# Optimization experiments

Hardware: AMD Instinct MI355X
Metric: run time of the kernel (lower is better)

## Reference

```python
import jax, jax.numpy as jnp
import numpy as np

HIDDEN = 1024
N_HEADS = 16
HEAD_DIM = HIDDEN // N_HEADS


def setup_inputs() -> dict:
    key = jax.random.key(0)
    ks = jax.random.split(key, 7)
    b, l, m = 4, 1024, 1024
    q = jax.random.normal(ks[0], (b, l, HIDDEN), dtype=jnp.float32)
    k = jax.random.normal(ks[1], (b, m, HIDDEN), dtype=jnp.float32)
    v = jax.random.normal(ks[2], (b, m, HIDDEN), dtype=jnp.float32)
    s = 1.0 / np.sqrt(HIDDEN)
    w_q = jax.random.normal(ks[3], (HIDDEN, HIDDEN), dtype=jnp.float32) * s
    w_k = jax.random.normal(ks[4], (HIDDEN, HIDDEN), dtype=jnp.float32) * s
    w_v = jax.random.normal(ks[5], (HIDDEN, HIDDEN), dtype=jnp.float32) * s
    w_o = jax.random.normal(ks[6], (HIDDEN, HIDDEN), dtype=jnp.float32) * s
    return {"q": q, "k": k, "v": v, "w_q": w_q, "w_k": w_k, "w_v": w_v, "w_o": w_o}


def reference(q, k, v, w_q, w_k, w_v, w_o):
    b, l, _ = q.shape
    _, m, _ = k.shape
    # Linear (bias=False): y = x @ W^T
    qp = q @ w_q.T
    kp = k @ w_k.T
    vp = v @ w_v.T  # projected but unused downstream (faithful to original bug)
    # Faithful non-standard split: hidden -> (head_dim, n_heads)
    qh = qp.reshape(b, l, HEAD_DIM, N_HEADS)
    kh = kp.reshape(b, m, HEAD_DIM, N_HEADS)
    # attn over K, scaled, softmax over m (dim=2)
    scores = jnp.einsum('bldn,bmdn->blmn', qh, kh) / np.sqrt(HEAD_DIM)
    attn = jax.nn.softmax(scores, axis=2)
    # dropout is identity in eval mode
    # NOTE: original attends over K (not V) — reproduced faithfully
    x = jnp.einsum('blmn,bmdn->bldn', attn, kh)
    x = x.reshape(b, l, HIDDEN)  # 'b l d n -> b l (d n)'
    return x @ w_o.T
```

## Files before the change

kernel.cpp:

```cpp
#include <hip/hip_runtime.h>
#include <hip/hip_bf16.h>
#include <stdint.h>
#include <math.h>


typedef __bf16 bf16;
typedef __bf16 bf16x8 __attribute__((ext_vector_type(8)));
typedef __bf16 bf16x4 __attribute__((ext_vector_type(4)));
typedef float  f32x4  __attribute__((ext_vector_type(4)));

__device__ __forceinline__ void async_load16(const void* g, void* l) {
  __builtin_amdgcn_global_load_lds((__attribute__((address_space(1))) void*)g,
                                   (__attribute__((address_space(3))) void*)l,
                                   16, 0, 0);
}

__device__ __forceinline__ void pipe_fence() {
  asm volatile("s_waitcnt vmcnt(0) lgkmcnt(0)" ::: "memory");
  __builtin_amdgcn_sched_barrier(0);
  __builtin_amdgcn_s_barrier();
}

__device__ __forceinline__ int detect_fl(const void* samp, int tid, int* smax) {
  int e = (((const unsigned short*)samp)[tid] >> 7) & 0xFF;
#pragma unroll
  for (int off = 1; off <= 32; off <<= 1) {
    int o = __shfl_xor(e, off);
    e = o > e ? o : e;
  }
  if ((tid & 63) == 0) smax[tid >> 6] = e;
  __syncthreads();
  int m01 = smax[0] > smax[1] ? smax[0] : smax[1];
  int m23 = smax[2] > smax[3] ? smax[2] : smax[3];
  return ((m01 > m23 ? m01 : m23) >= 140) ? 1 : 0;
}

__global__ void __launch_bounds__(256)
canon(const void* __restrict__ q, const void* __restrict__ k,
      const void* __restrict__ wq, const void* __restrict__ wk,
      const void* __restrict__ wo,
      bf16* __restrict__ qc, bf16* __restrict__ kc,
      bf16* __restrict__ wqc, bf16* __restrict__ wkc,
      bf16* __restrict__ wo_p, int* __restrict__ flag) {
  __shared__ int smax[4];
  const int tid = threadIdx.x;
  const int fl = detect_fl(q, tid, smax);
  if (blockIdx.x == 0 && tid == 0) *flag = fl;

  const size_t e0 = (size_t)blockIdx.x * 2048 + tid * 8;
  const size_t M4 = 4194304, M8 = 8388608, M9 = 9437184, M10 = 10485760;
  const void* src; bf16* dst; size_t le; bool perm = false;
  if (e0 < M4)       { src = q;  dst = qc;   le = e0;       }
  else if (e0 < M8)  { src = k;  dst = kc;   le = e0 - M4;  }
  else if (e0 < M9)  { src = wq; dst = wqc;  le = e0 - M8;  }
  else if (e0 < M10) { src = wk; dst = wkc;  le = e0 - M9;  }
  else               { src = wo; dst = wo_p; le = e0 - M10; perm = true; }

  if (!perm) {
    bf16x8 v;
    if (fl) {
      const float* p = (const float*)src + le;
      f32x4 a = *(const f32x4*)p, b = *(const f32x4*)(p + 4);
#pragma unroll
      for (int j = 0; j < 4; ++j) { v[j] = (bf16)a[j]; v[4 + j] = (bf16)b[j]; }
    } else {
      v = *(const bf16x8*)((const bf16*)src + le);
    }
    *(bf16x8*)(dst + le) = v;
  } else {
    int o = (int)(le >> 10), kp0 = (int)(le & 1023);
    bf16x8 v;
#pragma unroll
    for (int j = 0; j < 8; ++j) {
      int kp = kp0 + j;
      int h = ((kp & 63) << 4) | (kp >> 6);
      float f = fl ? ((const float*)src)[o * 1024 + h]
                   : (float)((const bf16*)src)[o * 1024 + h];
      f = fminf(fmaxf(f, -1024.f), 1024.f);
      v[j] = (bf16)f;
    }
    *(bf16x8*)(dst + le) = v;
  }
}

__global__ void __launch_bounds__(256, 3)
qk_gemm(const bf16* __restrict__ qc, const bf16* __restrict__ wqc,
        const bf16* __restrict__ kc, const bf16* __restrict__ wkc,
        bf16* __restrict__ qh, bf16* __restrict__ kh, bf16* __restrict__ khT,
        float cs) {
  __shared__ __align__(16) char smem[49152];
  bf16* const sA0 = (bf16*)smem;
  bf16* const sA1 = (bf16*)(smem + 16384);
  bf16* const sB0 = (bf16*)(smem + 32768);
  bf16* const sB1 = (bf16*)(smem + 40960);
  bf16* const epi = (bf16*)smem;

  const int tid  = threadIdx.x;
  const int lane = tid & 63;
  const int wave = tid >> 6;
  const int q4   = lane >> 4;
  const int c16  = lane & 15;
  const int wm   = wave >> 1;
  const int wn   = wave & 1;

  const int z = blockIdx.z;
  const bf16* A = z ? kc : qc;
  const bf16* W = z ? wkc : wqc;
  const float scale = z ? 1.0f : cs;
  bf16* out0 = z ? kh : qh;

  const int lin    = blockIdx.x + 8 * blockIdx.y;
  const int rowBlk = (lin & 31) * 128;
  const int colBlk = (lin >> 5) * 64;

  const bf16* gA[4]; int lA[4];
#pragma unroll
  for (int i = 0; i < 4; ++i) {
    int s = tid + 256 * i;
    int r = s >> 3, g = (s & 7) ^ (r & 7);
    gA[i] = A + (size_t)(rowBlk + r) * 1024 + g * 8;
    lA[i] = s * 8;
  }
  const bf16* gB[2]; int lB[2];
#pragma unroll
  for (int i = 0; i < 2; ++i) {
    int s = tid + 256 * i;
    int r = s >> 3, g = (s & 7) ^ (r & 7);
    gB[i] = W + (size_t)(colBlk + r) * 1024 + g * 8;
    lB[i] = s * 8;
  }

  f32x4 acc[4][2] = {};

#pragma unroll
  for (int i = 0; i < 4; ++i) async_load16(gA[i], sA0 + lA[i]);
#pragma unroll
  for (int i = 0; i < 2; ++i) async_load16(gB[i], sB0 + lB[i]);
  pipe_fence();

  for (int t = 0; t < 16; ++t) {
    if (t < 15) {
      const int kn = (t + 1) * 64;
      bf16* dA = (t & 1) ? sA0 : sA1;
      bf16* dB = (t & 1) ? sB0 : sB1;
#pragma unroll
      for (int i = 0; i < 4; ++i) async_load16(gA[i] + kn, dA + lA[i]);
#pragma unroll
      for (int i = 0; i < 2; ++i) async_load16(gB[i] + kn, dB + lB[i]);
    }

    const bf16* cA = (t & 1) ? sA1 : sA0;
    const bf16* cB = (t & 1) ? sB1 : sB0;
#pragma unroll
    for (int ks = 0; ks < 2; ++ks) {
      bf16x8 af[4], bfr[2];
#pragma unroll
      for (int mt = 0; mt < 4; ++mt) {
        int row = wm * 64 + mt * 16 + c16;
        af[mt] = *(const bf16x8*)(cA + row * 64 +
                   (((ks * 4 + q4) ^ (row & 7)) * 8));
      }
#pragma unroll
      for (int nt = 0; nt < 2; ++nt) {
        int row = wn * 32 + nt * 16 + c16;
        bfr[nt] = *(const bf16x8*)(cB + row * 64 +
                   (((ks * 4 + q4) ^ (row & 7)) * 8));
      }
#pragma unroll
      for (int mt = 0; mt < 4; ++mt)
#pragma unroll
        for (int nt = 0; nt < 2; ++nt)
          acc[mt][nt] = __builtin_amdgcn_mfma_f32_16x16x32_bf16(
              af[mt], bfr[nt], acc[mt][nt], 0, 0, 0);
    }
    pipe_fence();
  }

#pragma unroll
  for (int mt = 0; mt < 4; ++mt)
#pragma unroll
    for (int nt = 0; nt < 2; ++nt)
#pragma unroll
      for (int r = 0; r < 4; ++r) {
        int m_t = wm * 64 + mt * 16 + q4 * 4 + r;
        int c   = wn * 32 + nt * 16 + c16;
        epi[m_t * 70 + c] = (bf16)(acc[mt][nt][r] * scale);
      }
  __syncthreads();

  const int bb    = rowBlk >> 10;
  const int mbase = rowBlk & 1023;
  const int dg0   = colBlk >> 4;

  {
    int n = tid >> 4;
#pragma unroll
    for (int i = 0; i < 8; ++i) {
      int m_t = (tid & 15) + i * 16;
      bf16x4 v;
#pragma unroll
      for (int dt = 0; dt < 4; ++dt) v[dt] = epi[m_t * 70 + dt * 16 + n];
      *(bf16x4*)(out0 + ((size_t)(bb * 16 + n) * 1024 + mbase + m_t) * 64 + dg0) = v;
    }
  }
  if (z) {
    int r = tid >> 2, qtr = tid & 3;
    int n = r >> 2, dt = r & 3;
    int c = dt * 16 + n;
    size_t base = ((size_t)(bb * 16 + n) * 64 + dg0 + dt) * 1024 + mbase + qtr * 32;
#pragma unroll
    for (int c8 = 0; c8 < 4; ++c8) {
      bf16x8 v;
#pragma unroll
      for (int j = 0; j < 8; ++j) v[j] = epi[(qtr * 32 + c8 * 8 + j) * 70 + c];
      *(bf16x8*)(khT + base + c8 * 8) = v;
    }
  }
}

__global__ void __launch_bounds__(256, 3)
attn_kernel(const bf16* __restrict__ qh, const bf16* __restrict__ kh,
            const bf16* __restrict__ khT, bf16* __restrict__ xh) {
  __shared__ __align__(16) bf16 sK[2][64 * 64];
  __shared__ __align__(16) bf16 sKT[2][64 * 64];
  __shared__ __align__(16) bf16 sP[4][16 * 72];

  const int tid  = threadIdx.x;
  const int lane = tid & 63;
  const int wave = tid >> 6;
  const int q4   = lane >> 4;
  const int c16  = lane & 15;
  const int lin  = blockIdx.x;
  const int bn   = lin & 63;
  const int qt   = lin >> 6;
  const int b    = bn >> 4, n = bn & 15;
  const int l0w  = qt * 64 + wave * 16;

  const bf16* qhead  = qh  + (size_t)bn * (1024 * 64);
  const bf16* khead  = kh  + (size_t)bn * (1024 * 64);
  const bf16* kThead = khT + (size_t)bn * (64 * 1024);

  bf16x8 aq[2];
#pragma unroll
  for (int hh = 0; hh < 2; ++hh)
    aq[hh] = *(const bf16x8*)(qhead + (size_t)(l0w + c16) * 64 + hh * 32 + q4 * 8);

  int kr[2], kg[2];
#pragma unroll
  for (int i = 0; i < 2; ++i) {
    int s = tid + 256 * i;
    kr[i] = s >> 3;  kg[i] = (s & 7) ^ (kr[i] & 7);
  }

  f32x4 O[4] = {};
  f32x4 Osum = {};
  bf16x8 ones;
#pragma unroll
  for (int j = 0; j < 8; ++j) ones[j] = (bf16)1.0f;
  bf16* sPw = sP[wave];

#pragma unroll
  for (int i = 0; i < 2; ++i) {
    int s = (tid + 256 * i) * 8;
    async_load16(khead + (size_t)kr[i] * 64 + kg[i] * 8, &sK[0][s]);
    async_load16(kThead + (size_t)kr[i] * 1024 + kg[i] * 8, &sKT[0][s]);
  }
  pipe_fence();

  for (int t = 0; t < 16; ++t) {
    if (t < 15) {
      const int m0n = (t + 1) * 64;
      const int bi  = (t + 1) & 1;
#pragma unroll
      for (int i = 0; i < 2; ++i) {
        int s = (tid + 256 * i) * 8;
        async_load16(khead + (size_t)(m0n + kr[i]) * 64 + kg[i] * 8, &sK[bi][s]);
        async_load16(kThead + (size_t)kr[i] * 1024 + m0n + kg[i] * 8, &sKT[bi][s]);
      }
    }

    const bf16* cK  = sK[t & 1];
    const bf16* cKT = sKT[t & 1];

    f32x4 S[4] = {};
#pragma unroll
    for (int t4 = 0; t4 < 4; ++t4) {
#pragma unroll
      for (int hh = 0; hh < 2; ++hh) {
        int row = t4 * 16 + c16;
        bf16x8 bk = *(const bf16x8*)(cK + row * 64 +
                                     (((hh * 4 + q4) ^ (row & 7)) * 8));
        S[t4] = __builtin_amdgcn_mfma_f32_16x16x32_bf16(aq[hh], bk, S[t4], 0, 0, 0);
      }
    }

#pragma unroll
    for (int t4 = 0; t4 < 4; ++t4)
#pragma unroll
      for (int r = 0; r < 4; ++r) {
        float p = __builtin_amdgcn_exp2f(S[t4][r]);
        sPw[(q4 * 4 + r) * 72 + t4 * 16 + c16] = (bf16)p;
      }

    bf16x8 ap[2];
#pragma unroll
    for (int kk2 = 0; kk2 < 2; ++kk2) {
      ap[kk2] = *(const bf16x8*)(sPw + c16 * 72 + kk2 * 32 + q4 * 8);
      Osum = __builtin_amdgcn_mfma_f32_16x16x32_bf16(ap[kk2], ones, Osum, 0, 0, 0);
    }

#pragma unroll
    for (int td = 0; td < 4; ++td) {
#pragma unroll
      for (int kk2 = 0; kk2 < 2; ++kk2) {
        int row = td * 16 + c16;
        bf16x8 bkt = *(const bf16x8*)(cKT + row * 64 +
                                      (((kk2 * 4 + q4) ^ (row & 7)) * 8));
        O[td] = __builtin_amdgcn_mfma_f32_16x16x32_bf16(ap[kk2], bkt, O[td], 0, 0, 0);
      }
    }
    pipe_fence();
  }

  {
    float inv[4];
#pragma unroll
    for (int r = 0; r < 4; ++r) inv[r] = 1.0f / Osum[r];
#pragma unroll
    for (int td = 0; td < 4; ++td)
#pragma unroll
      for (int r = 0; r < 4; ++r)
        sPw[(q4 * 4 + r) * 72 + td * 16 + c16] = (bf16)(O[td][r] * inv[r]);
  }
  {
    int l_loc = lane >> 2, dq = lane & 3;
    bf16x8 v0 = *(const bf16x8*)(sPw + l_loc * 72 + dq * 16);
    bf16x8 v1 = *(const bf16x8*)(sPw + l_loc * 72 + dq * 16 + 8);
    size_t base = ((size_t)(b * 1024 + l0w + l_loc) * 16 + n) * 64 + dq * 16;
    *(bf16x8*)(xh + base)     = v0;
    *(bf16x8*)(xh + base + 8) = v1;
  }
}

__global__ void __launch_bounds__(256, 4)
o_gemm(const bf16* __restrict__ A, const bf16* __restrict__ W,
       bf16* __restrict__ out0, float* __restrict__ outf,
       const int* __restrict__ flag) {
  __shared__ __align__(16) bf16 sA[2][64 * 64];
  __shared__ __align__(16) bf16 sB[2][64 * 64];

  const int tid  = threadIdx.x;
  const int lane = tid & 63;
  const int wave = tid >> 6;
  const int q4   = lane >> 4;
  const int c16  = lane & 15;
  const int wm   = wave >> 1;
  const int wn   = wave & 1;

  const int lin    = blockIdx.x + 8 * blockIdx.y;
  const int rowBlk = (lin & 63) * 64;
  const int colBlk = (lin >> 6) * 64;

  const bf16* gA[2]; const bf16* gB[2]; int ls[2];
#pragma unroll
  for (int i = 0; i < 2; ++i) {
    int s = tid + 256 * i;
    int r = s >> 3, g = (s & 7) ^ (r & 7);
    gA[i] = A + (size_t)(rowBlk + r) * 1024 + g * 8;
    gB[i] = W + (size_t)(colBlk + r) * 1024 + g * 8;
    ls[i] = s * 8;
  }

  f32x4 acc[2][2] = {};

#pragma unroll
  for (int i = 0; i < 2; ++i) {
    async_load16(gA[i], &sA[0][ls[i]]);
    async_load16(gB[i], &sB[0][ls[i]]);
  }
  pipe_fence();

  for (int t = 0; t < 16; ++t) {
    if (t < 15) {
      const int kn = (t + 1) * 64;
      const int bi = (t + 1) & 1;
#pragma unroll
      for (int i = 0; i < 2; ++i) {
        async_load16(gA[i] + kn, &sA[bi][ls[i]]);
        async_load16(gB[i] + kn, &sB[bi][ls[i]]);
      }
    }

    const bf16* cA = sA[t & 1];
    const bf16* cB = sB[t & 1];
#pragma unroll
    for (int ks = 0; ks < 2; ++ks) {
      bf16x8 af[2], bfr[2];
#pragma unroll
      for (int mt = 0; mt < 2; ++mt) {
        int row = wm * 32 + mt * 16 + c16;
        af[mt] = *(const bf16x8*)(cA + row * 64 +
                   (((ks * 4 + q4) ^ (row & 7)) * 8));
      }
#pragma unroll
      for (int nt = 0; nt < 2; ++nt) {
        int row = wn * 32 + nt * 16 + c16;
        bfr[nt] = *(const bf16x8*)(cB + row * 64 +
                   (((ks * 4 + q4) ^ (row & 7)) * 8));
      }
#pragma unroll
      for (int mt = 0; mt < 2; ++mt)
#pragma unroll
        for (int nt = 0; nt < 2; ++nt)
          acc[mt][nt] = __builtin_amdgcn_mfma_f32_16x16x32_bf16(
              af[mt], bfr[nt], acc[mt][nt], 0, 0, 0);
    }
    pipe_fence();
  }

  const int fl = *flag;
#pragma unroll
  for (int mt = 0; mt < 2; ++mt)
#pragma unroll
    for (int nt = 0; nt < 2; ++nt)
#pragma unroll
      for (int r = 0; r < 4; ++r) {
        int gm = rowBlk + wm * 32 + mt * 16 + q4 * 4 + r;
        int gn = colBlk + wn * 32 + nt * 16 + c16;
        size_t idx = (size_t)gm * 1024 + gn;
        if (fl) outf[idx] = acc[mt][nt][r];
        else    out0[idx] = (bf16)acc[mt][nt][r];
      }
}

extern "C" void kernel_launch(void* const* d_in, const int* in_sizes, int n_in,
                              void* d_out, int out_size, void* d_ws, size_t ws_size,
                              hipStream_t stream) {
  const void* q_raw  = d_in[0];
  const void* k_raw  = d_in[1];
  const void* wq_raw = d_in[3];
  const void* wk_raw = d_in[4];
  const void* wo_raw = d_in[6];

  char* ws = (char*)d_ws;
  const size_t MB = 1024 * 1024;
  bf16* qc   = (bf16*)(ws + 0 * MB);
  bf16* kc   = (bf16*)(ws + 8 * MB);
  bf16* kh   = (bf16*)(ws + 16 * MB);
  bf16* wqc  = (bf16*)(ws + 24 * MB);
  bf16* wkc  = (bf16*)(ws + 26 * MB);
  bf16* wo_p = (bf16*)(ws + 28 * MB);
  int*  flag = (int*)(ws + 30 * MB);
  bf16* xh   = qc;
  bf16* qh   = (bf16*)d_out;
  bf16* khT  = (bf16*)((char*)d_out + 8 * MB);

  const float CS = 0.125f * 1.4426950408889634f;
  dim3 blk(256, 1, 1);

  hipLaunchKernelGGL(canon, dim3(5632), blk, 0, stream,
                     q_raw, k_raw, wq_raw, wk_raw, wo_raw,
                     qc, kc, wqc, wkc, wo_p, flag);
  hipLaunchKernelGGL(qk_gemm, dim3(8, 64, 2), blk, 0, stream,
                     qc, wqc, kc, wkc, qh, kh, khT, CS);
  hipLaunchKernelGGL(attn_kernel, dim3(1024), blk, 0, stream,
                     qh, kh, khT, xh);
  hipLaunchKernelGGL(o_gemm, dim3(8, 128), blk, 0, stream,
                     xh, wo_p, (bf16*)d_out, (float*)d_out, flag);
}
```

Baseline: 200.5 us.

## Use partial vmcnt waits so next-tile prefetch overlaps current-tile MFMA

Replaces the full vmcnt(0)+lgkmcnt(0) fence after each tile with a wait that only drains the previous tile's async LDS loads (vmcnt(N) after issuing the next prefetch), plus a separate lgkmcnt barrier at the end of the iteration. This lets global-to-LDS prefetch of tile t+1 stay in flight while tile t is computed, in the projection GEMM, attention and output GEMM kernels. The attention kernel also raises wave priority around MFMA blocks with s_setprio. This relies on the vmcnt counts exactly matching the number of outstanding loads issued per iteration.

```diff
diff --git a/kernel.cpp b/kernel.cpp
--- a/kernel.cpp
+++ b/kernel.cpp
@@ -15,10 +15,10 @@
                                    16, 0, 0);
 }
 
-__device__ __forceinline__ void pipe_fence() {
-  asm volatile("s_waitcnt vmcnt(0) lgkmcnt(0)" ::: "memory");
+__device__ __forceinline__ void join_pin() {
   __builtin_amdgcn_sched_barrier(0);
   __builtin_amdgcn_s_barrier();
+  __builtin_amdgcn_sched_barrier(0);
 }
 
 __device__ __forceinline__ int detect_fl(const void* samp, int tid, int* smax) {
@@ -136,7 +136,6 @@
   for (int i = 0; i < 4; ++i) async_load16(gA[i], sA0 + lA[i]);
 #pragma unroll
   for (int i = 0; i < 2; ++i) async_load16(gB[i], sB0 + lB[i]);
-  pipe_fence();
 
   for (int t = 0; t < 16; ++t) {
     if (t < 15) {
@@ -147,7 +146,11 @@
       for (int i = 0; i < 4; ++i) async_load16(gA[i] + kn, dA + lA[i]);
 #pragma unroll
       for (int i = 0; i < 2; ++i) async_load16(gB[i] + kn, dB + lB[i]);
-    }
+      asm volatile("s_waitcnt vmcnt(6)" ::: "memory");
+    } else {
+      asm volatile("s_waitcnt vmcnt(0)" ::: "memory");
+    }
+    join_pin();
 
     const bf16* cA = (t & 1) ? sA1 : sA0;
     const bf16* cB = (t & 1) ? sB1 : sB0;
@@ -173,7 +176,8 @@
           acc[mt][nt] = __builtin_amdgcn_mfma_f32_16x16x32_bf16(
               af[mt], bfr[nt], acc[mt][nt], 0, 0, 0);
     }
-    pipe_fence();
+    asm volatile("s_waitcnt lgkmcnt(0)" ::: "memory");
+    join_pin();
   }
 
 #pragma unroll
@@ -265,7 +269,6 @@
     async_load16(khead + (size_t)kr[i] * 64 + kg[i] * 8, &sK[0][s]);
     async_load16(kThead + (size_t)kr[i] * 1024 + kg[i] * 8, &sKT[0][s]);
   }
-  pipe_fence();
 
   for (int t = 0; t < 16; ++t) {
     if (t < 15) {
@@ -277,12 +280,17 @@
         async_load16(khead + (size_t)(m0n + kr[i]) * 64 + kg[i] * 8, &sK[bi][s]);
         async_load16(kThead + (size_t)kr[i] * 1024 + m0n + kg[i] * 8, &sKT[bi][s]);
       }
-    }
+      asm volatile("s_waitcnt vmcnt(4)" ::: "memory");
+    } else {
+      asm volatile("s_waitcnt vmcnt(0)" ::: "memory");
+    }
+    join_pin();
 
     const bf16* cK  = sK[t & 1];
     const bf16* cKT = sKT[t & 1];
 
     f32x4 S[4] = {};
+    __builtin_amdgcn_s_setprio(1);
 #pragma unroll
     for (int t4 = 0; t4 < 4; ++t4) {
 #pragma unroll
@@ -293,6 +301,7 @@
         S[t4] = __builtin_amdgcn_mfma_f32_16x16x32_bf16(aq[hh], bk, S[t4], 0, 0, 0);
       }
     }
+    __builtin_amdgcn_s_setprio(0);
 
 #pragma unroll
     for (int t4 = 0; t4 < 4; ++t4)
@@ -303,6 +312,7 @@
       }
 
     bf16x8 ap[2];
+    __builtin_amdgcn_s_setprio(1);
 #pragma unroll
     for (int kk2 = 0; kk2 < 2; ++kk2) {
       ap[kk2] = *(const bf16x8*)(sPw + c16 * 72 + kk2 * 32 + q4 * 8);
@@ -319,7 +329,9 @@
         O[td] = __builtin_amdgcn_mfma_f32_16x16x32_bf16(ap[kk2], bkt, O[td], 0, 0, 0);
       }
     }
-    pipe_fence();
+    __builtin_amdgcn_s_setprio(0);
+    asm volatile("s_waitcnt lgkmcnt(0)" ::: "memory");
+    join_pin();
   }
 
   {
@@ -378,7 +390,6 @@
     async_load16(gA[i], &sA[0][ls[i]]);
     async_load16(gB[i], &sB[0][ls[i]]);
   }
-  pipe_fence();
 
   for (int t = 0; t < 16; ++t) {
     if (t < 15) {
@@ -389,7 +400,11 @@
         async_load16(gA[i] + kn, &sA[bi][ls[i]]);
         async_load16(gB[i] + kn, &sB[bi][ls[i]]);
       }
-    }
+      asm volatile("s_waitcnt vmcnt(4)" ::: "memory");
+    } else {
+      asm volatile("s_waitcnt vmcnt(0)" ::: "memory");
+    }
+    join_pin();
 
     const bf16* cA = sA[t & 1];
     const bf16* cB = sB[t & 1];
@@ -415,7 +430,8 @@
           acc[mt][nt] = __builtin_amdgcn_mfma_f32_16x16x32_bf16(
               af[mt], bfr[nt], acc[mt][nt], 0, 0, 0);
     }
-    pipe_fence();
+    asm volatile("s_waitcnt lgkmcnt(0)" ::: "memory");
+    join_pin();
   }
 
   const int fl = *flag;
```

New measurement: 194.3 us. 3.1% less time.
